# Optimization experiments

Hardware: AMD Instinct MI355X
Metric: run time of the kernel (lower is better)

The kernel has to match this reference:

```python
import jax, jax.numpy as jnp
import numpy as np

OUT_FEATURES = 4096
IN_FEATURES = 16384
NNZ = 2_000_000
BATCH = 128


def setup_inputs() -> dict:
    key = jax.random.key(0)
    k1, k2, k3, k4, k5 = jax.random.split(key, 5)
    inputs = jax.random.normal(k1, (BATCH, IN_FEATURES), dtype=jnp.float32)
    # learned sparse weight values and bias (uniform init like reset_parameters)
    bound = 1.0 / (IN_FEATURES ** 0.5)
    values = jax.random.uniform(k2, (NNZ,), minval=-bound, maxval=bound, dtype=jnp.float32)
    bias = jax.random.uniform(k3, (OUT_FEATURES,), minval=-bound, maxval=bound, dtype=jnp.float32)
    # fixed COO connectivity: rows -> out_features, cols -> in_features
    rows = jax.random.randint(k4, (NNZ,), 0, OUT_FEATURES, dtype=jnp.int32)
    cols = jax.random.randint(k5, (NNZ,), 0, IN_FEATURES, dtype=jnp.int32)
    return {"inputs": inputs, "values": values, "bias": bias, "rows": rows, "cols": cols}


def reference(inputs, values, bias, rows, cols):
    # out[b, r] = sum_{k: rows[k]==r} values[k] * inputs[b, cols[k]]  (+ bias[r])
    # Gather input columns per nnz entry, scale, then scatter-add into output rows.
    contrib = inputs[:, cols] * values            # [B, nnz]
    out = jax.ops.segment_sum(contrib.T, rows, num_segments=OUT_FEATURES).T  # [B, out_features]
    return out + bias
```

## Files before the change

kernel.cpp:

```cpp
#include <hip/hip_runtime.h>
#include <hip/hip_fp16.h>

#define NNZ    2000000
#define BATCH  128
#define IN_F   16384
#define OUT_F  4096
#define NCH    512
#define CHUNK  3912
#define NBK    1024
#define RPB    4
#define BK_CAP 2240

__device__ inline int mbcnt64(unsigned long long m) {
  return __builtin_amdgcn_mbcnt_hi((unsigned)(m >> 32),
         __builtin_amdgcn_mbcnt_lo((unsigned)m, 0));
}


__global__ __launch_bounds__(512)
void k_localsort(const int* __restrict__ rows, const int* __restrict__ cols,
                 const float* __restrict__ vals, int* __restrict__ desc,
                 unsigned* __restrict__ pairs) {
  __shared__ unsigned stage[CHUNK];
  __shared__ int lrows[CHUNK];
  __shared__ int h[NBK], cur[NBK];
  __shared__ int wsums[8];
  const int t = threadIdx.x, c = blockIdx.x;
  const int lane = t & 63, w = t >> 6;
  const int base = c * CHUNK;
  const int n = min(CHUNK, NNZ - base);
  const int n4 = n >> 2;

  h[t] = 0; h[t + 512] = 0;
  __syncthreads();
  for (int i = t; i < n4; i += 512) {
    const int4 r4 = ((const int4*)(rows + base))[i];
    ((int4*)lrows)[i] = r4;
    atomicAdd(&h[r4.x >> 2], 1);
    atomicAdd(&h[r4.y >> 2], 1);
    atomicAdd(&h[r4.z >> 2], 1);
    atomicAdd(&h[r4.w >> 2], 1);
  }
  __syncthreads();
  const int v0 = h[2 * t], v1 = h[2 * t + 1];
  const int sv = v0 + v1;
  int x = sv;
#pragma unroll
  for (int off = 1; off < 64; off <<= 1) { int y = __shfl_up(x, off); if (lane >= off) x += y; }
  if (lane == 63) wsums[w] = x;
  __syncthreads();
  int wex = 0;
#pragma unroll
  for (int j = 0; j < 8; ++j) { const int sj = wsums[j]; wex += (j < w) ? sj : 0; }
  const int excl = wex + x - sv;
  cur[2 * t] = excl;
  cur[2 * t + 1] = excl + v0;
  ((int2*)desc)[c * 512 + t] = make_int2((excl << 8) | v0, ((excl + v0) << 8) | v1);
  __syncthreads();
  for (int i = t; i < n4; i += 512) {
    const int4   r4 = ((const int4*)lrows)[i];
    const int4   c4 = ((const int4*)(cols + base))[i];
    const float4 f4 = ((const float4*)(vals + base))[i];
    int pos;
    pos = atomicAdd(&cur[r4.x >> 2], 1);
    stage[pos] = ((unsigned)c4.x << 18) | ((unsigned)(r4.x & 3) << 16) | (unsigned)__half_as_ushort(__float2half(f4.x));
    pos = atomicAdd(&cur[r4.y >> 2], 1);
    stage[pos] = ((unsigned)c4.y << 18) | ((unsigned)(r4.y & 3) << 16) | (unsigned)__half_as_ushort(__float2half(f4.y));
    pos = atomicAdd(&cur[r4.z >> 2], 1);
    stage[pos] = ((unsigned)c4.z << 18) | ((unsigned)(r4.z & 3) << 16) | (unsigned)__half_as_ushort(__float2half(f4.z));
    pos = atomicAdd(&cur[r4.w >> 2], 1);
    stage[pos] = ((unsigned)c4.w << 18) | ((unsigned)(r4.w & 3) << 16) | (unsigned)__half_as_ushort(__float2half(f4.w));
  }
  __syncthreads();
  for (int j = t; j < n4; j += 512)
    ((uint4*)(pairs + base))[j] = ((const uint4*)stage)[j];
}

__global__ __launch_bounds__(256)
void k_mid(const int* __restrict__ desc, unsigned* __restrict__ rdesc,
           int* __restrict__ btot, const float* __restrict__ in,
           __half* __restrict__ inT) {
  __shared__ __align__(16) char smem[33280];
  const int t = threadIdx.x, lane = t & 63, w = t >> 6;

  if (blockIdx.x < 128) {
    int (*tl)[520] = (int (*)[520])smem;
    const int b0 = blockIdx.x * 8;
#pragma unroll
    for (int p = 0; p < 16; ++p) {
      const int idx = p * 256 + t;
      const int cc = idx >> 3, j = idx & 7;
      tl[j][cc] = desc[cc * NBK + b0 + j];
    }
    __syncthreads();
#pragma unroll
    for (int jj = 0; jj < 2; ++jj) {
      const int j = w + jj * 4;
      int carry = 0;
#pragma unroll
      for (int p = 0; p < 8; ++p) {
        const int cc = p * 64 + lane;
        const unsigned d = (unsigned)tl[j][cc];
        const int len = (int)(d & 255u);
        int x = len;
#pragma unroll
        for (int off = 1; off < 64; off <<= 1) { int y = __shfl_up(x, off); if (lane >= off) x += y; }
        rdesc[(b0 + j) * NCH + cc] = (d << 12) | (unsigned)(carry + x - len);
        carry += __shfl(x, 63);
      }
      if (lane == 0) btot[b0 + j] = carry;
    }
  } else {
    float* tileF = (float*)smem;
    const int c0 = (blockIdx.x - 128) * 64;
    const int q4 = t & 15, bq = t >> 4;
#pragma unroll
    for (int p = 0; p < 8; ++p) {
      const int b = p * 16 + bq;
      const float4 v = *(const float4*)(in + (size_t)b * IN_F + c0 + q4 * 4);
      float* dst = tileF + b * 65 + q4 * 4;
      dst[0] = v.x; dst[1] = v.y; dst[2] = v.z; dst[3] = v.w;
    }
    __syncthreads();
    const int oct = t & 15, cl0 = t >> 4;
#pragma unroll
    for (int p = 0; p < 4; ++p) {
      const int cl = p * 16 + cl0;
      const float* src = tileF + oct * 8 * 65 + cl;
      unsigned u0 = (unsigned)__half_as_ushort(__float2half(src[0]))
                  | ((unsigned)__half_as_ushort(__float2half(src[65])) << 16);
      unsigned u1 = (unsigned)__half_as_ushort(__float2half(src[130]))
                  | ((unsigned)__half_as_ushort(__float2half(src[195])) << 16);
      unsigned u2 = (unsigned)__half_as_ushort(__float2half(src[260]))
                  | ((unsigned)__half_as_ushort(__float2half(src[325])) << 16);
      unsigned u3 = (unsigned)__half_as_ushort(__float2half(src[390]))
                  | ((unsigned)__half_as_ushort(__float2half(src[455])) << 16);
      ((uint4*)inT)[(size_t)(c0 + cl) * 16 + oct] = make_uint4(u0, u1, u2, u3);
    }
  }
}

#define REFILL(SL, KK) do { \
    const int idx = (hh_ + 2 * (KK)) * 8 + 2 * g; \
    const bool vld = idx < nr; \
    const int i0_ = vld ? (s + idx) : 0; \
    uint2 pp = *((const uint2*)(sorted + i0_)); \
    if (!vld) { pp.x &= 0xffff0000u; pp.y &= 0xffff0000u; } \
    x##SL##0 = inT[(pp.x >> 18) * 16 + q]; \
    x##SL##1 = inT[(pp.y >> 18) * 16 + q]; \
    pv##SL = pp; \
  } while (0)

#define FMAH(SL) do { \
    const __half2 hv0 = __half2half2(__ushort_as_half((unsigned short)(pv##SL.x & 0xffffu))); \
    const __half2 hv1 = __half2half2(__ushort_as_half((unsigned short)(pv##SL.y & 0xffffu))); \
    const __half2* h0 = (const __half2*)&x##SL##0; \
    const __half2* h1 = (const __half2*)&x##SL##1; \
    hac0 = __hfma2(hv0, h0[0], hac0); hac1 = __hfma2(hv0, h0[1], hac1); \
    hac2 = __hfma2(hv0, h0[2], hac2); hac3 = __hfma2(hv0, h0[3], hac3); \
    hac0 = __hfma2(hv1, h1[0], hac0); hac1 = __hfma2(hv1, h1[1], hac1); \
    hac2 = __hfma2(hv1, h1[2], hac2); hac3 = __hfma2(hv1, h1[3], hac3); \
  } while (0)

#define STAGE(SL, NEXTKK) do { FMAH(SL); REFILL(SL, NEXTKK); } while (0)

#define FLUSH() do { \
    float2 f0 = __half22float2(hac0), f1 = __half22float2(hac1); \
    float2 f2 = __half22float2(hac2), f3 = __half22float2(hac3); \
    a0 += f0.x; a1 += f0.y; a2 += f1.x; a3 += f1.y; \
    a4 += f2.x; a5 += f2.y; a6 += f3.x; a7 += f3.y; \
    hac0 = hz; hac1 = hz; hac2 = hz; hac3 = hz; \
  } while (0)

__global__ __launch_bounds__(512, 8)
void k_spmm(const uint4* __restrict__ inT, const unsigned* __restrict__ pairs,
            const unsigned* __restrict__ rdesc, const int* __restrict__ btot,
            const float* __restrict__ bias, float* __restrict__ out) {
  __shared__ __align__(16) unsigned staging[BK_CAP];
  __shared__ __align__(16) unsigned sorted[BK_CAP + 8];
  __shared__ int  exd[NCH];
  __shared__ int  wrun[32];
  __shared__ unsigned long long wmask[32];
  __shared__ int  wcnt[32];
  __shared__ int  lst[RPB + 1];
  const int t = threadIdx.x, b = blockIdx.x;
  const int w = t >> 6, lane = t & 63;
  const int n = min(btot[b], BK_CAP);
  const int nrnd = (n + 511) & ~511;

  if (t < NCH) exd[t] = (int)rdesc[b * NCH + t];
  __syncthreads();
  for (int i = t; i < n; i += 512) {
    int lo = 0, hi = NCH - 1;
#pragma unroll
    for (int st = 0; st < 9; ++st) {
      const int mid = (lo + hi + 1) >> 1;
      if ((exd[mid] & 4095) <= i) lo = mid; else hi = mid - 1;
    }
    const unsigned d = (unsigned)exd[lo];
    staging[i] = pairs[lo * CHUNK + (int)(d >> 20) + (i - (int)(d & 4095u))];
  }
  __syncthreads();

  int cnt = 0;
  for (int i = w * 64 + lane; i < nrnd; i += 512) {
    const bool valid = i < n;
    const unsigned key = valid ? staging[i] : 0u;
    const int r4 = valid ? (int)((key >> 16) & 3u) : 4;
    unsigned long long m[4];
#pragma unroll
    for (int r = 0; r < 4; ++r) m[r] = __ballot(r4 == r);
    if (lane < 4) cnt += __popcll(m[lane]);
  }
  if (lane < 4) wcnt[w * 4 + lane] = cnt;
  __syncthreads();

  if (w == 0 && lane < 32) {
    const int v = wcnt[lane];
    int x = v;
#pragma unroll
    for (int off = 4; off < 32; off <<= 1) { int y = __shfl_up(x, off); if (lane >= off) x += y; }
    const int exw = x - v;
    int lstr = 0, tpad = 0;
#pragma unroll
    for (int rr = 0; rr < 4; ++rr) {
      const int tr = __shfl(x, 28 + rr);
      const int trE = (tr + 1) & ~1;
      if ((lane & 3) > rr) lstr += trE;
      tpad += trE;
    }
    wrun[lane] = lstr + exw;
    if (lane < 4) lst[lane] = lstr;
    if (lane == 0) lst[RPB] = tpad;
    if (lane >= 28) {
      if (x & 1) sorted[lstr + x] = 0u;
    }
  }
  __syncthreads();

  for (int i = w * 64 + lane; i < nrnd; i += 512) {
    const bool valid = i < n;
    const unsigned p = valid ? staging[i] : 0u;
    const int r4 = valid ? (int)((p >> 16) & 3u) : 4;
    unsigned long long m[4];
#pragma unroll
    for (int r = 0; r < 4; ++r) m[r] = __ballot(r4 == r);
    if (lane < 4) wmask[w * 4 + lane] = m[lane];
    if (valid) {
      const int rank = wrun[w * 4 + r4] + mbcnt64(wmask[w * 4 + r4]);
      sorted[rank] = p;
    }
    if (lane < 4) wrun[w * 4 + lane] += __popcll(m[lane]);
  }
  __syncthreads();

  const int rloc = w >> 1, hh_ = w & 1;
  const int r = b * RPB + rloc;
  const int g = lane >> 4, q = lane & 15;
  const int s = lst[rloc];
  const int nr = lst[rloc + 1] - s;
  const int nsteps = (nr + 7) >> 3;
  const int K = (nsteps + 1) >> 1;
  const int K3 = ((K + 2) / 3) * 3;

  float a0 = 0.f, a1 = 0.f, a2 = 0.f, a3 = 0.f, a4 = 0.f, a5 = 0.f, a6 = 0.f, a7 = 0.f;
  const __half2 hz = __float2half2_rn(0.f);
  __half2 hac0 = hz, hac1 = hz, hac2 = hz, hac3 = hz;
  uint4 xA0, xA1, xB0, xB1, xC0, xC1;
  uint2 pvA, pvB, pvC;

  REFILL(A, 0);
  REFILL(B, 1);
  REFILL(C, 2);
  for (int kk = 0; kk < K3; kk += 3) {
    STAGE(A, kk + 3);
    STAGE(B, kk + 4);
    STAGE(C, kk + 5);
    FLUSH();
  }

  a0 += __shfl_xor(a0, 16); a0 += __shfl_xor(a0, 32);
  a1 += __shfl_xor(a1, 16); a1 += __shfl_xor(a1, 32);
  a2 += __shfl_xor(a2, 16); a2 += __shfl_xor(a2, 32);
  a3 += __shfl_xor(a3, 16); a3 += __shfl_xor(a3, 32);
  a4 += __shfl_xor(a4, 16); a4 += __shfl_xor(a4, 32);
  a5 += __shfl_xor(a5, 16); a5 += __shfl_xor(a5, 32);
  a6 += __shfl_xor(a6, 16); a6 += __shfl_xor(a6, 32);
  a7 += __shfl_xor(a7, 16); a7 += __shfl_xor(a7, 32);

  float (*part)[BATCH] = (float (*)[BATCH])staging;
  if (hh_ == 1 && g == 0) {
    const int o = q * 8;
    part[rloc][o + 0] = a0; part[rloc][o + 1] = a1;
    part[rloc][o + 2] = a2; part[rloc][o + 3] = a3;
    part[rloc][o + 4] = a4; part[rloc][o + 5] = a5;
    part[rloc][o + 6] = a6; part[rloc][o + 7] = a7;
  }
  __syncthreads();
  if (hh_ == 0 && g == 0) {
    const float bs_ = bias[r];
    const int o = q * 8;
    out[(o + 0) * OUT_F + r] = a0 + part[rloc][o + 0] + bs_;
    out[(o + 1) * OUT_F + r] = a1 + part[rloc][o + 1] + bs_;
    out[(o + 2) * OUT_F + r] = a2 + part[rloc][o + 2] + bs_;
    out[(o + 3) * OUT_F + r] = a3 + part[rloc][o + 3] + bs_;
    out[(o + 4) * OUT_F + r] = a4 + part[rloc][o + 4] + bs_;
    out[(o + 5) * OUT_F + r] = a5 + part[rloc][o + 5] + bs_;
    out[(o + 6) * OUT_F + r] = a6 + part[rloc][o + 6] + bs_;
    out[(o + 7) * OUT_F + r] = a7 + part[rloc][o + 7] + bs_;
  }
}

extern "C" void kernel_launch(void* const* d_in, const int* in_sizes, int n_in,
                              void* d_out, int out_size, void* d_ws, size_t ws_size,
                              hipStream_t stream) {
  const float* inputs = (const float*)d_in[0];
  const float* values = (const float*)d_in[1];
  const float* bias   = (const float*)d_in[2];
  const int*   rows   = (const int*)d_in[3];
  const int*   cols   = (const int*)d_in[4];
  float* out = (float*)d_out;

  char* ws = (char*)d_ws;
  __half*   inputT = (__half*)(ws);
  unsigned* pairs  = (unsigned*)(ws + 4194304);
  int*      desc   = (int*)(ws + 12206080);
  unsigned* rdesc  = (unsigned*)(ws + 14303232);
  int*      btot   = (int*)(ws + 16400384);

  k_localsort<<<NCH, 512, 0, stream>>>(rows, cols, values, desc, pairs);
  k_mid      <<<384, 256, 0, stream>>>(desc, rdesc, btot, inputs, inputT);
  k_spmm     <<<NBK, 512, 0, stream>>>((const uint4*)inputT, pairs, rdesc, btot, bias, out);
}
```

Baseline: 122.3 us.

## Merge sort and transpose kernels, move bucket prefix scan into SpMM

Folds the input transpose/half-conversion into the local sort kernel as extra blocks and removes the middle kernel. Each SpMM block now computes its own per-chunk prefix scan over the 512 descriptors, replacing the precomputed rdesc/btot arrays. This drops a kernel launch and a global round-trip for the descriptors. In exchange the SpMM block does redundant scan work and strided loads of desc at its start.

```diff
diff --git a/kernel.cpp b/kernel.cpp
--- a/kernel.cpp
+++ b/kernel.cpp
@@ -18,114 +18,84 @@
 
 
 __global__ __launch_bounds__(512)
-void k_localsort(const int* __restrict__ rows, const int* __restrict__ cols,
-                 const float* __restrict__ vals, int* __restrict__ desc,
-                 unsigned* __restrict__ pairs) {
-  __shared__ unsigned stage[CHUNK];
-  __shared__ int lrows[CHUNK];
-  __shared__ int h[NBK], cur[NBK];
-  __shared__ int wsums[8];
-  const int t = threadIdx.x, c = blockIdx.x;
+void k_sort_tr(const int* __restrict__ rows, const int* __restrict__ cols,
+               const float* __restrict__ vals, int* __restrict__ desc,
+               unsigned* __restrict__ pairs, const float* __restrict__ in,
+               __half* __restrict__ inT) {
+  __shared__ __align__(16) char smem[39552];
+  const int t = threadIdx.x;
   const int lane = t & 63, w = t >> 6;
-  const int base = c * CHUNK;
-  const int n = min(CHUNK, NNZ - base);
-  const int n4 = n >> 2;
-
-  h[t] = 0; h[t + 512] = 0;
-  __syncthreads();
-  for (int i = t; i < n4; i += 512) {
-    const int4 r4 = ((const int4*)(rows + base))[i];
-    ((int4*)lrows)[i] = r4;
-    atomicAdd(&h[r4.x >> 2], 1);
-    atomicAdd(&h[r4.y >> 2], 1);
-    atomicAdd(&h[r4.z >> 2], 1);
-    atomicAdd(&h[r4.w >> 2], 1);
-  }
-  __syncthreads();
-  const int v0 = h[2 * t], v1 = h[2 * t + 1];
-  const int sv = v0 + v1;
-  int x = sv;
-#pragma unroll
-  for (int off = 1; off < 64; off <<= 1) { int y = __shfl_up(x, off); if (lane >= off) x += y; }
-  if (lane == 63) wsums[w] = x;
-  __syncthreads();
-  int wex = 0;
-#pragma unroll
-  for (int j = 0; j < 8; ++j) { const int sj = wsums[j]; wex += (j < w) ? sj : 0; }
-  const int excl = wex + x - sv;
-  cur[2 * t] = excl;
-  cur[2 * t + 1] = excl + v0;
-  ((int2*)desc)[c * 512 + t] = make_int2((excl << 8) | v0, ((excl + v0) << 8) | v1);
-  __syncthreads();
-  for (int i = t; i < n4; i += 512) {
-    const int4   r4 = ((const int4*)lrows)[i];
-    const int4   c4 = ((const int4*)(cols + base))[i];
-    const float4 f4 = ((const float4*)(vals + base))[i];
-    int pos;
-    pos = atomicAdd(&cur[r4.x >> 2], 1);
-    stage[pos] = ((unsigned)c4.x << 18) | ((unsigned)(r4.x & 3) << 16) | (unsigned)__half_as_ushort(__float2half(f4.x));
-    pos = atomicAdd(&cur[r4.y >> 2], 1);
-    stage[pos] = ((unsigned)c4.y << 18) | ((unsigned)(r4.y & 3) << 16) | (unsigned)__half_as_ushort(__float2half(f4.y));
-    pos = atomicAdd(&cur[r4.z >> 2], 1);
-    stage[pos] = ((unsigned)c4.z << 18) | ((unsigned)(r4.z & 3) << 16) | (unsigned)__half_as_ushort(__float2half(f4.z));
-    pos = atomicAdd(&cur[r4.w >> 2], 1);
-    stage[pos] = ((unsigned)c4.w << 18) | ((unsigned)(r4.w & 3) << 16) | (unsigned)__half_as_ushort(__float2half(f4.w));
-  }
-  __syncthreads();
-  for (int j = t; j < n4; j += 512)
-    ((uint4*)(pairs + base))[j] = ((const uint4*)stage)[j];
-}
-
-__global__ __launch_bounds__(256)
-void k_mid(const int* __restrict__ desc, unsigned* __restrict__ rdesc,
-           int* __restrict__ btot, const float* __restrict__ in,
-           __half* __restrict__ inT) {
-  __shared__ __align__(16) char smem[33280];
-  const int t = threadIdx.x, lane = t & 63, w = t >> 6;
-
-  if (blockIdx.x < 128) {
-    int (*tl)[520] = (int (*)[520])smem;
-    const int b0 = blockIdx.x * 8;
-#pragma unroll
-    for (int p = 0; p < 16; ++p) {
-      const int idx = p * 256 + t;
-      const int cc = idx >> 3, j = idx & 7;
-      tl[j][cc] = desc[cc * NBK + b0 + j];
-    }
-    __syncthreads();
-#pragma unroll
-    for (int jj = 0; jj < 2; ++jj) {
-      const int j = w + jj * 4;
-      int carry = 0;
-#pragma unroll
-      for (int p = 0; p < 8; ++p) {
-        const int cc = p * 64 + lane;
-        const unsigned d = (unsigned)tl[j][cc];
-        const int len = (int)(d & 255u);
-        int x = len;
-#pragma unroll
-        for (int off = 1; off < 64; off <<= 1) { int y = __shfl_up(x, off); if (lane >= off) x += y; }
-        rdesc[(b0 + j) * NCH + cc] = (d << 12) | (unsigned)(carry + x - len);
-        carry += __shfl(x, 63);
-      }
-      if (lane == 0) btot[b0 + j] = carry;
-    }
+
+  if (blockIdx.x < NCH) {
+    unsigned* stage = (unsigned*)smem;
+    int* lrows = (int*)(smem + 15648);
+    int* h     = (int*)(smem + 31296);
+    int* cur   = (int*)(smem + 35392);
+    int* wsums = (int*)(smem + 39488);
+    const int c = blockIdx.x;
+    const int base = c * CHUNK;
+    const int n = min(CHUNK, NNZ - base);
+    const int n4 = n >> 2;
+
+    h[t] = 0; h[t + 512] = 0;
+    __syncthreads();
+    for (int i = t; i < n4; i += 512) {
+      const int4 r4 = ((const int4*)(rows + base))[i];
+      ((int4*)lrows)[i] = r4;
+      atomicAdd(&h[r4.x >> 2], 1);
+      atomicAdd(&h[r4.y >> 2], 1);
+      atomicAdd(&h[r4.z >> 2], 1);
+      atomicAdd(&h[r4.w >> 2], 1);
+    }
+    __syncthreads();
+    const int v0 = h[2 * t], v1 = h[2 * t + 1];
+    const int sv = v0 + v1;
+    int x = sv;
+#pragma unroll
+    for (int off = 1; off < 64; off <<= 1) { int y = __shfl_up(x, off); if (lane >= off) x += y; }
+    if (lane == 63) wsums[w] = x;
+    __syncthreads();
+    int wex = 0;
+#pragma unroll
+    for (int j = 0; j < 8; ++j) { const int sj = wsums[j]; wex += (j < w) ? sj : 0; }
+    const int excl = wex + x - sv;
+    cur[2 * t] = excl;
+    cur[2 * t + 1] = excl + v0;
+    ((int2*)desc)[c * 512 + t] = make_int2((excl << 8) | v0, ((excl + v0) << 8) | v1);
+    __syncthreads();
+    for (int i = t; i < n4; i += 512) {
+      const int4   r4 = ((const int4*)lrows)[i];
+      const int4   c4 = ((const int4*)(cols + base))[i];
+      const float4 f4 = ((const float4*)(vals + base))[i];
+      int pos;
+      pos = atomicAdd(&cur[r4.x >> 2], 1);
+      stage[pos] = ((unsigned)c4.x << 18) | ((unsigned)(r4.x & 3) << 16) | (unsigned)__half_as_ushort(__float2half(f4.x));
+      pos = atomicAdd(&cur[r4.y >> 2], 1);
+      stage[pos] = ((unsigned)c4.y << 18) | ((unsigned)(r4.y & 3) << 16) | (unsigned)__half_as_ushort(__float2half(f4.y));
+      pos = atomicAdd(&cur[r4.z >> 2], 1);
+      stage[pos] = ((unsigned)c4.z << 18) | ((unsigned)(r4.z & 3) << 16) | (unsigned)__half_as_ushort(__float2half(f4.z));
+      pos = atomicAdd(&cur[r4.w >> 2], 1);
+      stage[pos] = ((unsigned)c4.w << 18) | ((unsigned)(r4.w & 3) << 16) | (unsigned)__half_as_ushort(__float2half(f4.w));
+    }
+    __syncthreads();
+    for (int j = t; j < n4; j += 512)
+      ((uint4*)(pairs + base))[j] = ((const uint4*)stage)[j];
   } else {
     float* tileF = (float*)smem;
-    const int c0 = (blockIdx.x - 128) * 64;
-    const int q4 = t & 15, bq = t >> 4;
-#pragma unroll
-    for (int p = 0; p < 8; ++p) {
-      const int b = p * 16 + bq;
-      const float4 v = *(const float4*)(in + (size_t)b * IN_F + c0 + q4 * 4);
-      float* dst = tileF + b * 65 + q4 * 4;
+    const int c0 = (blockIdx.x - NCH) * 64;
+#pragma unroll
+    for (int p = 0; p < 4; ++p) {
+      const int idx = p * 512 + t;
+      const int b = idx >> 4, q = idx & 15;
+      const float4 v = *(const float4*)(in + (size_t)b * IN_F + c0 + q * 4);
+      float* dst = tileF + b * 65 + q * 4;
       dst[0] = v.x; dst[1] = v.y; dst[2] = v.z; dst[3] = v.w;
     }
     __syncthreads();
-    const int oct = t & 15, cl0 = t >> 4;
-#pragma unroll
-    for (int p = 0; p < 4; ++p) {
-      const int cl = p * 16 + cl0;
+#pragma unroll
+    for (int p = 0; p < 2; ++p) {
+      const int idx = p * 512 + t;
+      const int cl = idx >> 4, oct = idx & 15;
       const float* src = tileF + oct * 8 * 65 + cl;
       unsigned u0 = (unsigned)__half_as_ushort(__float2half(src[0]))
                   | ((unsigned)__half_as_ushort(__float2half(src[65])) << 16);
@@ -174,8 +144,8 @@
 
 __global__ __launch_bounds__(512, 8)
 void k_spmm(const uint4* __restrict__ inT, const unsigned* __restrict__ pairs,
-            const unsigned* __restrict__ rdesc, const int* __restrict__ btot,
-            const float* __restrict__ bias, float* __restrict__ out) {
+            const int* __restrict__ desc, const float* __restrict__ bias,
+            float* __restrict__ out) {
   __shared__ __align__(16) unsigned staging[BK_CAP];
   __shared__ __align__(16) unsigned sorted[BK_CAP + 8];
   __shared__ int  exd[NCH];
@@ -183,13 +153,29 @@
   __shared__ unsigned long long wmask[32];
   __shared__ int  wcnt[32];
   __shared__ int  lst[RPB + 1];
+  __shared__ int  wsum8[8];
+  __shared__ int  nsh;
   const int t = threadIdx.x, b = blockIdx.x;
   const int w = t >> 6, lane = t & 63;
-  const int n = min(btot[b], BK_CAP);
+
+  {
+    const unsigned d = (unsigned)desc[t * NBK + b];
+    const int len = (int)(d & 255u);
+    int x = len;
+#pragma unroll
+    for (int off = 1; off < 64; off <<= 1) { int y = __shfl_up(x, off); if (lane >= off) x += y; }
+    if (lane == 63) wsum8[w] = x;
+    __syncthreads();
+    int pre = 0;
+#pragma unroll
+    for (int j = 0; j < 8; ++j) { const int sj = wsum8[j]; pre += (j < w) ? sj : 0; }
+    exd[t] = (int)((d << 12) | (unsigned)(pre + x - len));
+    if (t == 511) nsh = pre + x;
+  }
+  __syncthreads();
+  const int n = min(nsh, BK_CAP);
   const int nrnd = (n + 511) & ~511;
 
-  if (t < NCH) exd[t] = (int)rdesc[b * NCH + t];
-  __syncthreads();
   for (int i = t; i < n; i += 512) {
     int lo = 0, hi = NCH - 1;
 #pragma unroll
@@ -325,10 +311,7 @@
   __half*   inputT = (__half*)(ws);
   unsigned* pairs  = (unsigned*)(ws + 4194304);
   int*      desc   = (int*)(ws + 12206080);
-  unsigned* rdesc  = (unsigned*)(ws + 14303232);
-  int*      btot   = (int*)(ws + 16400384);
-
-  k_localsort<<<NCH, 512, 0, stream>>>(rows, cols, values, desc, pairs);
-  k_mid      <<<384, 256, 0, stream>>>(desc, rdesc, btot, inputs, inputT);
-  k_spmm     <<<NBK, 512, 0, stream>>>((const uint4*)inputT, pairs, rdesc, btot, bias, out);
+
+  k_sort_tr<<<NCH + 256, 512, 0, stream>>>(rows, cols, values, desc, pairs, inputs, inputT);
+  k_spmm   <<<NBK,       512, 0, stream>>>((const uint4*)inputT, pairs, desc, bias, out);
 }
```

After: 118.9 us. 1.03x faster.
